# Performance work log

Measured on AMD Instinct MI355X. Metric: run time of the kernel, lower is better.

The kernel has to match this reference:

```python
import jax, jax.numpy as jnp
import numpy as np

N_INP = 1024
N_HID = 1024
N_OUT = 1024
B, S = 8, 2048


def setup_inputs() -> dict:
    key = jax.random.key(0)
    ks = jax.random.split(key, 9)
    s_in = 1.0 / np.sqrt(N_INP)
    s_hid = 1.0 / np.sqrt(N_HID)
    return {
        "x": jax.random.normal(ks[0], (B, S, N_INP), jnp.float32),
        "wq": jax.random.uniform(ks[1], (N_INP, N_HID), jnp.float32, -s_in, s_in),
        "bq": jax.random.uniform(ks[2], (N_HID,), jnp.float32, -s_in, s_in),
        "wk": jax.random.uniform(ks[3], (N_INP, N_HID), jnp.float32, -s_in, s_in),
        "bk": jax.random.uniform(ks[4], (N_HID,), jnp.float32, -s_in, s_in),
        "wv": jax.random.uniform(ks[5], (N_INP, N_HID), jnp.float32, -s_in, s_in),
        "bv": jax.random.uniform(ks[6], (N_HID,), jnp.float32, -s_in, s_in),
        "wo": jax.random.uniform(ks[7], (N_HID, N_OUT), jnp.float32, -s_hid, s_hid),
        "bo": jax.random.uniform(ks[8], (N_OUT,), jnp.float32, -s_hid, s_hid),
    }


def reference(x, wq, bq, wk, bk, wv, bv, wo, bo):
    # x: [B, S, n_inp]
    q = jnp.einsum("bsi,ih->bsh", x, wq) + bq  # [B,S,H]
    k = jnp.einsum("bsi,ih->bsh", x, wk) + bk
    v = jnp.einsum("bsi,ih->bsh", x, wv) + bv
    scale = 1.0 / jnp.sqrt(jnp.float32(N_HID))
    energy = jnp.einsum("bqh,bkh->bqk", q, k) * scale  # [B,S,S]
    attn = jax.nn.softmax(energy, axis=-1)  # dropout=0.0 (eval)
    ctx = jnp.einsum("bqk,bkh->bqh", attn, v)  # [B,S,H]
    out = jnp.einsum("bsh,ho->bso", ctx, wo) + bo  # [B,S,n_out]
    return out
```

## Files before the change

kernel.cpp:

```cpp
#include <hip/hip_runtime.h>
#include <hip/hip_bf16.h>


typedef __attribute__((ext_vector_type(8))) __bf16 bf16x8;
typedef __attribute__((ext_vector_type(4))) __bf16 bf16x4;
typedef __attribute__((ext_vector_type(4))) float  f32x4;
typedef __attribute__((ext_vector_type(8))) float  f32x8;

__device__ __forceinline__ void gl_lds16(const void* g, void* l) {
    __builtin_amdgcn_global_load_lds(
        (__attribute__((address_space(1))) const void*)g,
        (__attribute__((address_space(3))) void*)l, 16, 0, 0);
}

template <bool SWP>
__device__ __forceinline__ f32x4 mfma16(bf16x8 a, bf16x8 b, f32x4 c) {
    if constexpr (SWP)
        return __builtin_amdgcn_mfma_f32_16x16x32_bf16(b, a, c, 0, 0, 0);
    else
        return __builtin_amdgcn_mfma_f32_16x16x32_bf16(a, b, c, 0, 0, 0);
}

__global__ __launch_bounds__(256) void k_prep(
    const float* __restrict__ x,
    const float* __restrict__ w0, const float* __restrict__ w1,
    const float* __restrict__ w2, const float* __restrict__ w3,
    const float* __restrict__ bq, const float* __restrict__ bk,
    const float* __restrict__ bv,
    __bf16* __restrict__ Xb, __bf16* __restrict__ WT, float* __restrict__ bc) {
    __shared__ float tsh[64][65];
    const int bid = blockIdx.x, tid = threadIdx.x;
    if (bid < 8192) {
        const int i = bid * 256 + tid;
        f32x8 a = *((const f32x8*)x + i);
        bf16x8 o;
#pragma unroll
        for (int j = 0; j < 8; ++j) o[j] = (__bf16)a[j];
        *((bf16x8*)Xb + i) = o;
    } else if (bid < 9216) {
        const int tt = bid - 8192;
        const int z = tt >> 8, rem = tt & 255;
        const int bx = (rem & 15) * 64, by = (rem >> 4) * 64;
        const float* W = (z == 0) ? w0 : (z == 1) ? w1 : (z == 2) ? w2 : w3;
        __bf16* Wo = WT + (long long)z * 1048576;
        const int c4 = (tid & 15) * 4, r0 = tid >> 4;
#pragma unroll
        for (int p = 0; p < 4; ++p) {
            const int r = r0 + p * 16;
            f32x4 v = *(const f32x4*)(W + (long long)(by + r) * 1024 + bx + c4);
#pragma unroll
            for (int j = 0; j < 4; ++j) tsh[r][c4 + j] = v[j];
        }
        __syncthreads();
#pragma unroll
        for (int p = 0; p < 4; ++p) {
            const int r = r0 + p * 16;
            bf16x4 o;
#pragma unroll
            for (int j = 0; j < 4; ++j) o[j] = (__bf16)tsh[c4 + j][r];
            *(bf16x4*)(Wo + (long long)(bx + r) * 1024 + by + c4) = o;
        }
    } else {
        const int i = (bid - 9216) * 256 + tid;
        const float* s = (i < 1024) ? bq : (i < 2048 ? bk : bv);
        bc[i] = s[i & 1023];
    }
}

__global__ __launch_bounds__(512) void k_softmax(__bf16* __restrict__ E) {
    const int tid = threadIdx.x;
    const int half = tid >> 8, t = tid & 255;
    __bf16* p = E + ((long long)blockIdx.x * 2 + half) * 2048;
    const int l = tid & 63, w4 = (tid >> 6) & 3;
    bf16x8 vb = *((const bf16x8*)p + t);
    float v[8];
#pragma unroll
    for (int i = 0; i < 8; ++i) v[i] = (float)vb[i];
    float m = v[0];
#pragma unroll
    for (int i = 1; i < 8; ++i) m = fmaxf(m, v[i]);
    for (int off = 32; off > 0; off >>= 1) m = fmaxf(m, __shfl_xor(m, off));
    __shared__ float redm[2][4], reds[2][4];
    if (l == 0) redm[half][w4] = m;
    __syncthreads();
    m = fmaxf(fmaxf(redm[half][0], redm[half][1]),
              fmaxf(redm[half][2], redm[half][3]));
    float e[8], s = 0.f;
#pragma unroll
    for (int i = 0; i < 8; ++i) { e[i] = __expf(v[i] - m); s += e[i]; }
    for (int off = 32; off > 0; off >>= 1) s += __shfl_xor(s, off);
    if (l == 0) reds[half][w4] = s;
    __syncthreads();
    s = reds[half][0] + reds[half][1] + reds[half][2] + reds[half][3];
    const float inv = 1.0f / s;
    bf16x8 o;
#pragma unroll
    for (int i = 0; i < 8; ++i) o[i] = (__bf16)(e[i] * inv);
    *((bf16x8*)p + t) = o;
}

template <int MODE, bool HAS_BIAS>
__global__ __launch_bounds__(512, 2) void gemm_bt(
    const __bf16* __restrict__ A, const __bf16* __restrict__ Bt,
    const float* __restrict__ bias, void* __restrict__ Cout,
    int K, int lda, int ldb, int ldc, int gy, int rpx, int bnc,
    float scale, long long sA, long long sB, long long sC) {
    constexpr bool SWP = (MODE != 4);
    __shared__ __align__(16) __bf16 Abuf0[16384];
    __shared__ __align__(16) __bf16 Bbuf0[16384];
    __shared__ __align__(16) __bf16 Abuf1[16384];
    __shared__ __align__(16) __bf16 Bbuf1[16384];

    const int lid = blockIdx.x;
    const int xcd = lid & 7;
    const int jj = lid >> 3;
    const int bn = jj % bnc;
    const int rt = xcd * rpx + jj / bnc;
    const int z = rt / gy;
    const int bm = rt - z * gy;

    const __bf16* Ab = A + (long long)z * sA;
    const __bf16* Bb = Bt + (long long)z * sB;

    const int tid = threadIdx.x;
    const int l = tid & 63, w = tid >> 6;
    const int wm = w >> 2, wn = w & 3;

    const int rA = tid >> 3;
    const int cswz = (tid & 7) ^ (rA & 7);
    const __bf16* aSg = Ab + (long long)(bm * 256 + rA) * lda + cswz * 8;
    const __bf16* bSg = Bb + (long long)(bn * 256 + rA) * ldb + cswz * 8;
    const long long a64 = (long long)lda * 64;
    const long long b64 = (long long)ldb * 64;
    const int ldst = tid * 16;

    const int r16 = l & 15, kq4 = l >> 4;
    const int sw0 = kq4 ^ (r16 & 7);
    const int aro0 = (wm * 128 + r16) * 64 + sw0 * 8;
    const int aro1 = aro0 ^ 32;
    const int bro0 = (wn * 64 + r16) * 64 + sw0 * 8;
    const int bro1 = bro0 ^ 32;

    f32x4 acc[8][4] = {};
    bf16x8 bf[4][2];

#define ST_A(buf, j, t)                                                    \
    gl_lds16(aSg + (j) * a64 + (long long)(t) * 64,                        \
             (char*)(buf) + ldst + (j) * 8192)
#define ST_B(buf, j, t)                                                    \
    gl_lds16(bSg + (j) * b64 + (long long)(t) * 64,                        \
             (char*)(buf) + ldst + (j) * 8192)

#define RD_B(buf)                                                          \
    do {                                                                   \
        _Pragma("unroll") for (int ni = 0; ni < 4; ++ni) {                 \
            bf[ni][0] = *(const bf16x8*)((buf) + bro0 + ni * 1024);        \
            bf[ni][1] = *(const bf16x8*)((buf) + bro1 + ni * 1024);        \
        }                                                                  \
    } while (0)

#define BARR                                                               \
    do {                                                                   \
        __builtin_amdgcn_sched_barrier(0);                                 \
        __builtin_amdgcn_s_barrier();                                      \
        __builtin_amdgcn_sched_barrier(0);                                 \
    } while (0)
#define WV4 asm volatile("s_waitcnt vmcnt(4)" ::: "memory")
#define WV0 asm volatile("s_waitcnt vmcnt(0)" ::: "memory")
#define NOW ((void)0)
#define TS4 do { WV4; BARR; } while (0)
#define TS0 do { WV0; BARR; } while (0)

#define PHASE(Abuf, p, RB, RBUF, STAGES, TAILOP)                               \
    do {                                                                      \
        STAGES;                                                               \
        bf16x8 af0k0 = *(const bf16x8*)((Abuf) + aro0 + (2 * (p)) * 1024);     \
        bf16x8 af0k1 = *(const bf16x8*)((Abuf) + aro1 + (2 * (p)) * 1024);     \
        bf16x8 af1k0 = *(const bf16x8*)((Abuf) + aro0 + (2 * (p) + 1) * 1024); \
        bf16x8 af1k1 = *(const bf16x8*)((Abuf) + aro1 + (2 * (p) + 1) * 1024); \
        if (RB) RD_B(RBUF);                                                   \
        BARR;                                                                 \
        __builtin_amdgcn_s_setprio(1);                                        \
        _Pragma("unroll") for (int ni = 0; ni < 4; ++ni) {                    \
            acc[2 * (p)][ni] = mfma16<SWP>(af0k0, bf[ni][0], acc[2*(p)][ni]); \
            acc[2 * (p)][ni] = mfma16<SWP>(af0k1, bf[ni][1], acc[2*(p)][ni]); \
            acc[2*(p)+1][ni] = mfma16<SWP>(af1k0, bf[ni][0], acc[2*(p)+1][ni]);\
            acc[2*(p)+1][ni] = mfma16<SWP>(af1k1, bf[ni][1], acc[2*(p)+1][ni]);\
        }                                                                     \
        __builtin_amdgcn_s_setprio(0);                                        \
        TAILOP;                                                               \
    } while (0)

    ST_B(Bbuf0, 0, 0); ST_B(Bbuf0, 1, 0); ST_B(Bbuf0, 2, 0); ST_B(Bbuf0, 3, 0);
    ST_A(Abuf0, 0, 0); ST_A(Abuf0, 1, 0); ST_A(Abuf0, 2, 0); ST_A(Abuf0, 3, 0);
    ST_B(Bbuf1, 0, 1); ST_B(Bbuf1, 1, 1); ST_B(Bbuf1, 2, 1); ST_B(Bbuf1, 3, 1);
    WV4;
    BARR;

    const int NT = K >> 6;
    for (int t0 = 0; t0 + 3 < NT; t0 += 2) {
        PHASE(Abuf0, 0, 1, Bbuf0,
              (ST_A(Abuf1, 0, t0 + 1), ST_A(Abuf1, 1, t0 + 1),
               ST_A(Abuf1, 2, t0 + 1), ST_A(Abuf1, 3, t0 + 1)), NOW);
        PHASE(Abuf0, 1, 0, Bbuf0, NOW, NOW);
        PHASE(Abuf0, 2, 0, Bbuf0,
              (ST_B(Bbuf0, 0, t0 + 2), ST_B(Bbuf0, 1, t0 + 2)), NOW);
        PHASE(Abuf0, 3, 0, Bbuf0,
              (ST_B(Bbuf0, 2, t0 + 2), ST_B(Bbuf0, 3, t0 + 2)), TS4);
        PHASE(Abuf1, 0, 1, Bbuf1,
              (ST_A(Abuf0, 0, t0 + 2), ST_A(Abuf0, 1, t0 + 2)), NOW);
        PHASE(Abuf1, 1, 0, Bbuf1,
              (ST_A(Abuf0, 2, t0 + 2), ST_A(Abuf0, 3, t0 + 2)), NOW);
        PHASE(Abuf1, 2, 0, Bbuf1,
              (ST_B(Bbuf1, 0, t0 + 3), ST_B(Bbuf1, 1, t0 + 3)), NOW);
        PHASE(Abuf1, 3, 0, Bbuf1,
              (ST_B(Bbuf1, 2, t0 + 3), ST_B(Bbuf1, 3, t0 + 3)), TS4);
    }
    {
        PHASE(Abuf0, 0, 1, Bbuf0,
              (ST_A(Abuf1, 0, NT - 1), ST_A(Abuf1, 1, NT - 1),
               ST_A(Abuf1, 2, NT - 1), ST_A(Abuf1, 3, NT - 1)), NOW);
        PHASE(Abuf0, 1, 0, Bbuf0, NOW, NOW);
        PHASE(Abuf0, 2, 0, Bbuf0, NOW, NOW);
        PHASE(Abuf0, 3, 0, Bbuf0, NOW, TS0);
        PHASE(Abuf1, 0, 1, Bbuf1, NOW, NOW);
        PHASE(Abuf1, 1, 0, Bbuf1, NOW, NOW);
        PHASE(Abuf1, 2, 0, Bbuf1, NOW, NOW);
        PHASE(Abuf1, 3, 0, Bbuf1, NOW, NOW);
    }
#undef ST_A
#undef ST_B
#undef RD_B
#undef BARR
#undef WV4
#undef WV0
#undef NOW
#undef TS4
#undef TS0
#undef PHASE

    const int quad = kq4;
    if constexpr (MODE == 2) {
        __bf16* Qb = (__bf16*)Cout;
        const int part = bn >> 2;
#pragma unroll
        for (int mi = 0; mi < 8; ++mi) {
            const int srow0 = bm * 256 + wm * 128 + mi * 16 + r16;
            const int b = srow0 >> 11;
            const int s0 = srow0 & 2047;
#pragma unroll
            for (int ni = 0; ni < 4; ++ni) {
                const int col0 = bn * 256 + wn * 64 + ni * 16 + quad * 4;
                const f32x4 bb = *(const f32x4*)(bias + col0);
                const int c1 = col0 - part * 1024;
                bf16x4 o;
#pragma unroll
                for (int rr = 0; rr < 4; ++rr) o[rr] = (__bf16)(acc[mi][ni][rr] + bb[rr]);
                *(bf16x4*)(Qb + (long long)part * 16777216 +
                           (long long)b * 2097152 + (long long)s0 * 1024 + c1) = o;
            }
        }
    } else if constexpr (MODE == 4) {
        __bf16* Vb = (__bf16*)Cout;
#pragma unroll
        for (int mi = 0; mi < 8; ++mi) {
            const int srow0 = bm * 256 + wm * 128 + mi * 16 + quad * 4;
            const int b = srow0 >> 11;
            const int s0 = srow0 & 2047;
#pragma unroll
            for (int ni = 0; ni < 4; ++ni) {
                const int c1 = bn * 256 + wn * 64 + ni * 16 + r16;
                const float bb = HAS_BIAS ? bias[c1] : 0.0f;
                bf16x4 o;
#pragma unroll
                for (int rr = 0; rr < 4; ++rr) o[rr] = (__bf16)(acc[mi][ni][rr] + bb);
                *(bf16x4*)(Vb + (long long)b * 2097152 +
                           (long long)c1 * 2048 + s0) = o;
            }
        }
    } else {
        const long long cbase = (long long)z * sC;
#pragma unroll
        for (int mi = 0; mi < 8; ++mi) {
            const int row = bm * 256 + wm * 128 + mi * 16 + r16;
#pragma unroll
            for (int ni = 0; ni < 4; ++ni) {
                const int col0 = bn * 256 + wn * 64 + ni * 16 + quad * 4;
                f32x4 v;
                if constexpr (HAS_BIAS) {
                    const f32x4 bb = *(const f32x4*)(bias + col0);
#pragma unroll
                    for (int rr = 0; rr < 4; ++rr) v[rr] = acc[mi][ni][rr] * scale + bb[rr];
                } else {
#pragma unroll
                    for (int rr = 0; rr < 4; ++rr) v[rr] = acc[mi][ni][rr] * scale;
                }
                if constexpr (MODE == 1) {
                    *(f32x4*)((float*)Cout + cbase + (long long)row * ldc + col0) = v;
                } else {
                    bf16x4 o;
#pragma unroll
                    for (int rr = 0; rr < 4; ++rr) o[rr] = (__bf16)v[rr];
                    *(bf16x4*)((__bf16*)Cout + cbase + (long long)row * ldc + col0) = o;
                }
            }
        }
    }
}

extern "C" void kernel_launch(void* const* d_in, const int* in_sizes, int n_in,
                              void* d_out, int out_size, void* d_ws, size_t ws_size,
                              hipStream_t stream) {
    const float* x  = (const float*)d_in[0];
    const float* wq = (const float*)d_in[1];
    const float* bq = (const float*)d_in[2];
    const float* wk = (const float*)d_in[3];
    const float* bk = (const float*)d_in[4];
    const float* wv = (const float*)d_in[5];
    const float* bv = (const float*)d_in[6];
    const float* wo = (const float*)d_in[7];
    const float* bo = (const float*)d_in[8];
    float* out = (float*)d_out;

    __bf16* ws  = (__bf16*)d_ws;
    __bf16* Xb  = ws;
    __bf16* E   = ws;
    __bf16* Q   = ws + 33554432;
    __bf16* Kb  = ws + 50331648;
    __bf16* Vt  = ws + 67108864;
    __bf16* Ctx = ws + 83886080;
    __bf16* WT  = ws + 100663296;
    float*  bc  = (float*)(ws + 104857600);

    k_prep<<<9228, 256, 0, stream>>>(x, wq, wk, wv, wo, bq, bk, bv, Xb, WT, bc);

    gemm_bt<2, true><<<512, 512, 0, stream>>>(
        Xb, WT, bc, Q, 1024, 1024, 1024, 0, 64, 8, 8, 1.0f, 0, 0, 0);

    gemm_bt<4, true><<<256, 512, 0, stream>>>(
        Xb, WT + 2097152, bc + 2048, Vt, 1024, 1024, 1024, 0, 64, 8, 4,
        1.0f, 0, 0, 0);

    gemm_bt<0, false><<<512, 512, 0, stream>>>(
        Q, Kb, nullptr, E, 1024, 1024, 1024, 2048, 8, 8, 8,
        0.03125f, 2097152, 2097152, 4194304);

    k_softmax<<<8192, 512, 0, stream>>>(E);

    gemm_bt<0, false><<<256, 512, 0, stream>>>(
        E, Vt, nullptr, Ctx, 2048, 2048, 2048, 1024, 8, 8, 4,
        1.0f, 4194304, 2097152, 2097152);

    gemm_bt<1, true><<<256, 512, 0, stream>>>(
        Ctx, WT + 3145728, bo, out, 1024, 1024, 1024, 1024, 64, 8, 4,
        1.0f, 0, 0, 0);
}
```

Measured before the change: 441.8 us.

## Use 4-wave 256x256 GEMM tiles with 128x128 per-wave subtiles

The GEMM kernel drops from 8 waves of 512 threads to 4 waves of 256 threads. Each wave now computes a 128x128 subtile with 64 accumulators, which doubles register-level reuse of LDS fragments. The fine-grained 8-phase interleaved staging schedule is replaced by a simpler per-tile double buffer: it issues all loads for the next tile, computes the current one with software-prefetched A fragments, then waits with vmcnt(0) and a barrier. This raises register pressure and lowers occupancy to one block per CU, so the coarser sync may expose more memory latency.

After: 516.6 us. 1.17x slower.

```diff
diff --git a/kernel.cpp b/kernel.cpp
--- a/kernel.cpp
+++ b/kernel.cpp
@@ -100,7 +100,7 @@
 }
 
 template <int MODE, bool HAS_BIAS>
-__global__ __launch_bounds__(512, 2) void gemm_bt(
+__global__ __launch_bounds__(256, 1) void gemm_bt(
     const __bf16* __restrict__ A, const __bf16* __restrict__ Bt,
     const float* __restrict__ bias, void* __restrict__ Cout,
     int K, int lda, int ldb, int ldc, int gy, int rpx, int bnc,
@@ -124,120 +124,108 @@
 
     const int tid = threadIdx.x;
     const int l = tid & 63, w = tid >> 6;
-    const int wm = w >> 2, wn = w & 3;
+    const int wm = w >> 1, wn = w & 1;
 
     const int rA = tid >> 3;
     const int cswz = (tid & 7) ^ (rA & 7);
     const __bf16* aSg = Ab + (long long)(bm * 256 + rA) * lda + cswz * 8;
     const __bf16* bSg = Bb + (long long)(bn * 256 + rA) * ldb + cswz * 8;
-    const long long a64 = (long long)lda * 64;
-    const long long b64 = (long long)ldb * 64;
+    const long long a32 = (long long)lda * 32;
+    const long long b32 = (long long)ldb * 32;
     const int ldst = tid * 16;
 
     const int r16 = l & 15, kq4 = l >> 4;
     const int sw0 = kq4 ^ (r16 & 7);
     const int aro0 = (wm * 128 + r16) * 64 + sw0 * 8;
     const int aro1 = aro0 ^ 32;
-    const int bro0 = (wn * 64 + r16) * 64 + sw0 * 8;
+    const int bro0 = (wn * 128 + r16) * 64 + sw0 * 8;
     const int bro1 = bro0 ^ 32;
 
-    f32x4 acc[8][4] = {};
-    bf16x8 bf[4][2];
-
-#define ST_A(buf, j, t)                                                    \
-    gl_lds16(aSg + (j) * a64 + (long long)(t) * 64,                        \
-             (char*)(buf) + ldst + (j) * 8192)
-#define ST_B(buf, j, t)                                                    \
-    gl_lds16(bSg + (j) * b64 + (long long)(t) * 64,                        \
-             (char*)(buf) + ldst + (j) * 8192)
-
-#define RD_B(buf)                                                          \
-    do {                                                                   \
-        _Pragma("unroll") for (int ni = 0; ni < 4; ++ni) {                 \
+    f32x4 acc[8][8] = {};
+    bf16x8 bf[8][2];
+    bf16x8 sAk00, sAk01, sAk10, sAk11;
+    bf16x8 tAk00, tAk01, tAk10, tAk11;
+
+#define STAGE16(bufA, bufB, t)                                             \
+    do {                                                                   \
+        _Pragma("unroll") for (int j = 0; j < 8; ++j)                      \
+            gl_lds16(aSg + j * a32 + (long long)(t) * 64,                  \
+                     (char*)(bufA) + ldst + j * 4096);                     \
+        _Pragma("unroll") for (int j = 0; j < 8; ++j)                      \
+            gl_lds16(bSg + j * b32 + (long long)(t) * 64,                  \
+                     (char*)(bufB) + ldst + j * 4096);                     \
+    } while (0)
+
+#define RD_B16(buf)                                                        \
+    do {                                                                   \
+        _Pragma("unroll") for (int ni = 0; ni < 8; ++ni) {                 \
             bf[ni][0] = *(const bf16x8*)((buf) + bro0 + ni * 1024);        \
             bf[ni][1] = *(const bf16x8*)((buf) + bro1 + ni * 1024);        \
         }                                                                  \
     } while (0)
 
+#define PRA(N, buf, np)                                                    \
+    do {                                                                   \
+        N##k00 = *(const bf16x8*)((buf) + aro0 + (2 * (np)) * 1024);       \
+        N##k01 = *(const bf16x8*)((buf) + aro1 + (2 * (np)) * 1024);       \
+        N##k10 = *(const bf16x8*)((buf) + aro0 + (2 * (np) + 1) * 1024);   \
+        N##k11 = *(const bf16x8*)((buf) + aro1 + (2 * (np) + 1) * 1024);   \
+    } while (0)
+
+#define MM32(pp, U)                                                          \
+    do {                                                                     \
+        __builtin_amdgcn_s_setprio(1);                                       \
+        _Pragma("unroll") for (int ni = 0; ni < 8; ++ni)                     \
+            acc[2*(pp)][ni] = mfma16<SWP>(U##k00, bf[ni][0], acc[2*(pp)][ni]);\
+        _Pragma("unroll") for (int ni = 0; ni < 8; ++ni)                     \
+            acc[2*(pp)+1][ni] = mfma16<SWP>(U##k10, bf[ni][0], acc[2*(pp)+1][ni]);\
+        _Pragma("unroll") for (int ni = 0; ni < 8; ++ni)                     \
+            acc[2*(pp)][ni] = mfma16<SWP>(U##k01, bf[ni][1], acc[2*(pp)][ni]);\
+        _Pragma("unroll") for (int ni = 0; ni < 8; ++ni)                     \
+            acc[2*(pp)+1][ni] = mfma16<SWP>(U##k11, bf[ni][1], acc[2*(pp)+1][ni]);\
+        __builtin_amdgcn_s_setprio(0);                                       \
+    } while (0)
+
 #define BARR                                                               \
     do {                                                                   \
         __builtin_amdgcn_sched_barrier(0);                                 \
         __builtin_amdgcn_s_barrier();                                      \
         __builtin_amdgcn_sched_barrier(0);                                 \
     } while (0)
-#define WV4 asm volatile("s_waitcnt vmcnt(4)" ::: "memory")
 #define WV0 asm volatile("s_waitcnt vmcnt(0)" ::: "memory")
-#define NOW ((void)0)
-#define TS4 do { WV4; BARR; } while (0)
-#define TS0 do { WV0; BARR; } while (0)
-
-#define PHASE(Abuf, p, RB, RBUF, STAGES, TAILOP)                               \
-    do {                                                                      \
-        STAGES;                                                               \
-        bf16x8 af0k0 = *(const bf16x8*)((Abuf) + aro0 + (2 * (p)) * 1024);     \
-        bf16x8 af0k1 = *(const bf16x8*)((Abuf) + aro1 + (2 * (p)) * 1024);     \
-        bf16x8 af1k0 = *(const bf16x8*)((Abuf) + aro0 + (2 * (p) + 1) * 1024); \
-        bf16x8 af1k1 = *(const bf16x8*)((Abuf) + aro1 + (2 * (p) + 1) * 1024); \
-        if (RB) RD_B(RBUF);                                                   \
-        BARR;                                                                 \
-        __builtin_amdgcn_s_setprio(1);                                        \
-        _Pragma("unroll") for (int ni = 0; ni < 4; ++ni) {                    \
-            acc[2 * (p)][ni] = mfma16<SWP>(af0k0, bf[ni][0], acc[2*(p)][ni]); \
-            acc[2 * (p)][ni] = mfma16<SWP>(af0k1, bf[ni][1], acc[2*(p)][ni]); \
-            acc[2*(p)+1][ni] = mfma16<SWP>(af1k0, bf[ni][0], acc[2*(p)+1][ni]);\
-            acc[2*(p)+1][ni] = mfma16<SWP>(af1k1, bf[ni][1], acc[2*(p)+1][ni]);\
-        }                                                                     \
-        __builtin_amdgcn_s_setprio(0);                                        \
-        TAILOP;                                                               \
-    } while (0)
-
-    ST_B(Bbuf0, 0, 0); ST_B(Bbuf0, 1, 0); ST_B(Bbuf0, 2, 0); ST_B(Bbuf0, 3, 0);
-    ST_A(Abuf0, 0, 0); ST_A(Abuf0, 1, 0); ST_A(Abuf0, 2, 0); ST_A(Abuf0, 3, 0);
-    ST_B(Bbuf1, 0, 1); ST_B(Bbuf1, 1, 1); ST_B(Bbuf1, 2, 1); ST_B(Bbuf1, 3, 1);
-    WV4;
+
+#define TILE(Ac, Bc, An, Bn, tn, DOSTAGE)                                  \
+    do {                                                                   \
+        if (DOSTAGE) STAGE16(An, Bn, tn);                                  \
+        RD_B16(Bc);                                                        \
+        PRA(sA, Ac, 0);                                                    \
+        PRA(tA, Ac, 1); MM32(0, sA);                                       \
+        PRA(sA, Ac, 2); MM32(1, tA);                                       \
+        PRA(tA, Ac, 3); MM32(2, sA);                                       \
+        MM32(3, tA);                                                       \
+        if (DOSTAGE) WV0;                                                  \
+        BARR;                                                              \
+    } while (0)
+
+    STAGE16(Abuf0, Bbuf0, 0);
+    WV0;
     BARR;
 
     const int NT = K >> 6;
-    for (int t0 = 0; t0 + 3 < NT; t0 += 2) {
-        PHASE(Abuf0, 0, 1, Bbuf0,
-              (ST_A(Abuf1, 0, t0 + 1), ST_A(Abuf1, 1, t0 + 1),
-               ST_A(Abuf1, 2, t0 + 1), ST_A(Abuf1, 3, t0 + 1)), NOW);
-        PHASE(Abuf0, 1, 0, Bbuf0, NOW, NOW);
-        PHASE(Abuf0, 2, 0, Bbuf0,
-              (ST_B(Bbuf0, 0, t0 + 2), ST_B(Bbuf0, 1, t0 + 2)), NOW);
-        PHASE(Abuf0, 3, 0, Bbuf0,
-              (ST_B(Bbuf0, 2, t0 + 2), ST_B(Bbuf0, 3, t0 + 2)), TS4);
-        PHASE(Abuf1, 0, 1, Bbuf1,
-              (ST_A(Abuf0, 0, t0 + 2), ST_A(Abuf0, 1, t0 + 2)), NOW);
-        PHASE(Abuf1, 1, 0, Bbuf1,
-              (ST_A(Abuf0, 2, t0 + 2), ST_A(Abuf0, 3, t0 + 2)), NOW);
-        PHASE(Abuf1, 2, 0, Bbuf1,
-              (ST_B(Bbuf1, 0, t0 + 3), ST_B(Bbuf1, 1, t0 + 3)), NOW);
-        PHASE(Abuf1, 3, 0, Bbuf1,
-              (ST_B(Bbuf1, 2, t0 + 3), ST_B(Bbuf1, 3, t0 + 3)), TS4);
+    int t0 = 0;
+    for (; t0 + 3 < NT; t0 += 2) {
+        TILE(Abuf0, Bbuf0, Abuf1, Bbuf1, t0 + 1, true);
+        TILE(Abuf1, Bbuf1, Abuf0, Bbuf0, t0 + 2, true);
     }
-    {
-        PHASE(Abuf0, 0, 1, Bbuf0,
-              (ST_A(Abuf1, 0, NT - 1), ST_A(Abuf1, 1, NT - 1),
-               ST_A(Abuf1, 2, NT - 1), ST_A(Abuf1, 3, NT - 1)), NOW);
-        PHASE(Abuf0, 1, 0, Bbuf0, NOW, NOW);
-        PHASE(Abuf0, 2, 0, Bbuf0, NOW, NOW);
-        PHASE(Abuf0, 3, 0, Bbuf0, NOW, TS0);
-        PHASE(Abuf1, 0, 1, Bbuf1, NOW, NOW);
-        PHASE(Abuf1, 1, 0, Bbuf1, NOW, NOW);
-        PHASE(Abuf1, 2, 0, Bbuf1, NOW, NOW);
-        PHASE(Abuf1, 3, 0, Bbuf1, NOW, NOW);
-    }
-#undef ST_A
-#undef ST_B
-#undef RD_B
+    TILE(Abuf0, Bbuf0, Abuf1, Bbuf1, NT - 1, true);
+    TILE(Abuf1, Bbuf1, Abuf0, Bbuf0, 0, false);
+#undef STAGE16
+#undef RD_B16
+#undef PRA
+#undef MM32
 #undef BARR
-#undef WV4
 #undef WV0
-#undef NOW
-#undef TS4
-#undef TS0
-#undef PHASE
+#undef TILE
 
     const int quad = kq4;
     if constexpr (MODE == 2) {
@@ -249,8 +237,8 @@
             const int b = srow0 >> 11;
             const int s0 = srow0 & 2047;
 #pragma unroll
-            for (int ni = 0; ni < 4; ++ni) {
-                const int col0 = bn * 256 + wn * 64 + ni * 16 + quad * 4;
+            for (int ni = 0; ni < 8; ++ni) {
+                const int col0 = bn * 256 + wn * 128 + ni * 16 + quad * 4;
                 const f32x4 bb = *(const f32x4*)(bias + col0);
                 const int c1 = col0 - part * 1024;
                 bf16x4 o;
@@ -268,8 +256,8 @@
             const int b = srow0 >> 11;
             const int s0 = srow0 & 2047;
 #pragma unroll
-            for (int ni = 0; ni < 4; ++ni) {
-                const int c1 = bn * 256 + wn * 64 + ni * 16 + r16;
+            for (int ni = 0; ni < 8; ++ni) {
+                const int c1 = bn * 256 + wn * 128 + ni * 16 + r16;
                 const float bb = HAS_BIAS ? bias[c1] : 0.0f;
                 bf16x4 o;
 #pragma unroll
@@ -284,8 +272,8 @@
         for (int mi = 0; mi < 8; ++mi) {
             const int row = bm * 256 + wm * 128 + mi * 16 + r16;
 #pragma unroll
-            for (int ni = 0; ni < 4; ++ni) {
-                const int col0 = bn * 256 + wn * 64 + ni * 16 + quad * 4;
+            for (int ni = 0; ni < 8; ++ni) {
+                const int col0 = bn * 256 + wn * 128 + ni * 16 + quad * 4;
                 f32x4 v;
                 if constexpr (HAS_BIAS) {
                     const f32x4 bb = *(const f32x4*)(bias + col0);
@@ -334,24 +322,24 @@
 
     k_prep<<<9228, 256, 0, stream>>>(x, wq, wk, wv, wo, bq, bk, bv, Xb, WT, bc);
 
-    gemm_bt<2, true><<<512, 512, 0, stream>>>(
+    gemm_bt<2, true><<<512, 256, 0, stream>>>(
         Xb, WT, bc, Q, 1024, 1024, 1024, 0, 64, 8, 8, 1.0f, 0, 0, 0);
 
-    gemm_bt<4, true><<<256, 512, 0, stream>>>(
+    gemm_bt<4, true><<<256, 256, 0, stream>>>(
         Xb, WT + 2097152, bc + 2048, Vt, 1024, 1024, 1024, 0, 64, 8, 4,
         1.0f, 0, 0, 0);
 
-    gemm_bt<0, false><<<512, 512, 0, stream>>>(
+    gemm_bt<0, false><<<512, 256, 0, stream>>>(
         Q, Kb, nullptr, E, 1024, 1024, 1024, 2048, 8, 8, 8,
         0.03125f, 2097152, 2097152, 4194304);
 
     k_softmax<<<8192, 512, 0, stream>>>(E);
 
-    gemm_bt<0, false><<<256, 512, 0, stream>>>(
+    gemm_bt<0, false><<<256, 256, 0, stream>>>(
         E, Vt, nullptr, Ctx, 2048, 2048, 2048, 1024, 8, 8, 4,
         1.0f, 4194304, 2097152, 2097152);
 
-    gemm_bt<1, true><<<256, 512, 0, stream>>>(
+    gemm_bt<1, true><<<256, 256, 0, stream>>>(
         Ctx, WT + 3145728, bo, out, 1024, 1024, 1024, 1024, 64, 8, 4,
         1.0f, 0, 0, 0);
 }
```
